# Kernel tuning notes

Measured on AMD Instinct MI355X. Metric: run time of the kernel, lower is better.

The kernel has to match this reference:

```python
import jax, jax.numpy as jnp
import numpy as np

BETA = 0.99
THRESHOLD = 1.0
NUM_STEPS = 100
BATCH = 131072

# snntorch heaviside spike with ATan surrogate gradient (alpha=2 default)
@jax.custom_vjp
def spike(x):
    return (x > 0).astype(x.dtype)

def _spike_fwd(x):
    return (x > 0).astype(x.dtype), x

def _spike_bwd(x, g):
    # d/dx atan surrogate, alpha=2: 1 / (1 + (pi * x)^2)
    return (g / (1.0 + (jnp.pi * x) ** 2),)

spike.defvjp(_spike_fwd, _spike_bwd)


def setup_inputs() -> dict:
    key = jax.random.key(0)
    k = jax.random.split(key, 5)
    x = jax.random.normal(k[0], (BATCH, 2), dtype=jnp.float32)
    # Linear params, fan_in = 2 -> init scale ~ 1/sqrt(2) like torch default
    s = 1.0 / np.sqrt(2.0)
    W1 = jax.random.uniform(k[1], (2, 2), jnp.float32, -s, s)
    b1 = jax.random.uniform(k[2], (2,), jnp.float32, -s, s)
    W2 = jax.random.uniform(k[3], (2, 2), jnp.float32, -s, s)
    b2 = jax.random.uniform(k[4], (2,), jnp.float32, -s, s)
    return {"x": x, "W1": W1, "b1": b1, "W2": W2, "b2": b2}


def reference(x, W1, b1, W2, b2):
    # cur1 = fc1(x) is identical every step; compute once (same math as loop).
    cur1 = x @ W1.T + b1  # [B, 2]

    def lif(mem, cur):
        # snntorch Leaky, reset_mechanism='subtract':
        # reset from PREVIOUS mem (detached), then integrate, then fire.
        reset = jax.lax.stop_gradient((mem - THRESHOLD > 0).astype(mem.dtype))
        mem = BETA * mem + cur - reset * THRESHOLD
        spk = spike(mem - THRESHOLD)
        return spk, mem

    def step(carry, _):
        mem1, mem2 = carry
        spk1, mem1 = lif(mem1, cur1)
        cur2 = spk1 @ W2.T + b2
        spk2, mem2 = lif(mem2, cur2)
        return (mem1, mem2), (spk2, mem2)

    mem0 = jnp.zeros_like(cur1)
    _, (spk2_rec, mem2_rec) = jax.lax.scan(
        step, (mem0, mem0), None, length=NUM_STEPS
    )
    return spk2_rec, mem2_rec  # each [NUM_STEPS, B, 2]
```

## Files before the change

### kernel.cpp

```cpp
#include <hip/hip_runtime.h>

#define BATCH 131072
#define STEPS 100

__global__ __launch_bounds__(256) void snn_lif_kernel(
    const float* __restrict__ x,
    const float* __restrict__ W1, const float* __restrict__ b1,
    const float* __restrict__ W2, const float* __restrict__ b2,
    float* __restrict__ out)
{
    const int tid = blockIdx.x * blockDim.x + threadIdx.x;

    const float w100 = W1[0], w101 = W1[1], w110 = W1[2], w111 = W1[3];
    const float b10  = b1[0], b11  = b1[1];
    const float w200 = W2[0], w201 = W2[1], w210 = W2[2], w211 = W2[3];
    const float b20  = b2[0], b21  = b2[1];

    const float4 xv = reinterpret_cast<const float4*>(x)[tid];

    const float c1a0 = xv.x * w100 + xv.y * w101 + b10;
    const float c1a1 = xv.x * w110 + xv.y * w111 + b11;
    const float c1b0 = xv.z * w100 + xv.w * w101 + b10;
    const float c1b1 = xv.z * w110 + xv.w * w111 + b11;

    float m1a0 = 0.f, m1a1 = 0.f, m1b0 = 0.f, m1b1 = 0.f;
    float m2a0 = 0.f, m2a1 = 0.f, m2b0 = 0.f, m2b1 = 0.f;

    float4* __restrict__ spk_out = reinterpret_cast<float4*>(out);
    float4* __restrict__ mem_out =
        reinterpret_cast<float4*>(out + (size_t)STEPS * BATCH * 2);

    const int slab = BATCH / 2;

#pragma unroll 4
    for (int t = 0; t < STEPS; ++t) {
        float r, s1a0, s1a1, s1b0, s1b1;

        r = (m1a0 > 1.0f) ? 1.0f : 0.0f;
        m1a0 = 0.99f * m1a0 + c1a0 - r;
        s1a0 = (m1a0 > 1.0f) ? 1.0f : 0.0f;

        r = (m1a1 > 1.0f) ? 1.0f : 0.0f;
        m1a1 = 0.99f * m1a1 + c1a1 - r;
        s1a1 = (m1a1 > 1.0f) ? 1.0f : 0.0f;

        r = (m1b0 > 1.0f) ? 1.0f : 0.0f;
        m1b0 = 0.99f * m1b0 + c1b0 - r;
        s1b0 = (m1b0 > 1.0f) ? 1.0f : 0.0f;

        r = (m1b1 > 1.0f) ? 1.0f : 0.0f;
        m1b1 = 0.99f * m1b1 + c1b1 - r;
        s1b1 = (m1b1 > 1.0f) ? 1.0f : 0.0f;

        const float c2a0 = s1a0 * w200 + s1a1 * w201 + b20;
        const float c2a1 = s1a0 * w210 + s1a1 * w211 + b21;
        const float c2b0 = s1b0 * w200 + s1b1 * w201 + b20;
        const float c2b1 = s1b0 * w210 + s1b1 * w211 + b21;

        float4 sp;

        r = (m2a0 > 1.0f) ? 1.0f : 0.0f;
        m2a0 = 0.99f * m2a0 + c2a0 - r;
        sp.x = (m2a0 > 1.0f) ? 1.0f : 0.0f;

        r = (m2a1 > 1.0f) ? 1.0f : 0.0f;
        m2a1 = 0.99f * m2a1 + c2a1 - r;
        sp.y = (m2a1 > 1.0f) ? 1.0f : 0.0f;

        r = (m2b0 > 1.0f) ? 1.0f : 0.0f;
        m2b0 = 0.99f * m2b0 + c2b0 - r;
        sp.z = (m2b0 > 1.0f) ? 1.0f : 0.0f;

        r = (m2b1 > 1.0f) ? 1.0f : 0.0f;
        m2b1 = 0.99f * m2b1 + c2b1 - r;
        sp.w = (m2b1 > 1.0f) ? 1.0f : 0.0f;

        const float4 mm = make_float4(m2a0, m2a1, m2b0, m2b1);

        spk_out[(size_t)t * slab + tid] = sp;
        mem_out[(size_t)t * slab + tid] = mm;
    }
}

extern "C" void kernel_launch(void* const* d_in, const int* in_sizes, int n_in,
                              void* d_out, int out_size, void* d_ws, size_t ws_size,
                              hipStream_t stream) {
    const float* x  = (const float*)d_in[0];
    const float* W1 = (const float*)d_in[1];
    const float* b1 = (const float*)d_in[2];
    const float* W2 = (const float*)d_in[3];
    const float* b2 = (const float*)d_in[4];
    float* out = (float*)d_out;

    const int threads = 256;
    const int blocks = (BATCH / 2) / threads;
    snn_lif_kernel<<<blocks, threads, 0, stream>>>(x, W1, b1, W2, b2, out);
}
```

Before: 35.86 us.

## Split time steps into windows across grid y with recomputed warm-up prefix

The time dimension is split into four windows mapped to blockIdx.y. Each block recomputes the recurrence from step zero up to its window start without storing anything, then writes outputs only for its own window. This quadruples the block count (256 blocks to 1024) so the GPU is filled better and more stores are in flight, at the cost of redundant recurrence compute, up to 75 extra steps for the last window.

```diff
diff --git a/kernel.cpp b/kernel.cpp
--- a/kernel.cpp
+++ b/kernel.cpp
@@ -2,6 +2,42 @@
 
 #define BATCH 131072
 #define STEPS 100
+#define WINDOWS 4
+#define WLEN (STEPS / WINDOWS)
+
+
+#define LIF_STEP()                                                   \
+    do {                                                             \
+        float r, s1a0, s1a1, s1b0, s1b1;                             \
+        r = (m1a0 > 1.0f) ? 1.0f : 0.0f;                             \
+        m1a0 = 0.99f * m1a0 + c1a0 - r;                              \
+        s1a0 = (m1a0 > 1.0f) ? 1.0f : 0.0f;                          \
+        r = (m1a1 > 1.0f) ? 1.0f : 0.0f;                             \
+        m1a1 = 0.99f * m1a1 + c1a1 - r;                              \
+        s1a1 = (m1a1 > 1.0f) ? 1.0f : 0.0f;                          \
+        r = (m1b0 > 1.0f) ? 1.0f : 0.0f;                             \
+        m1b0 = 0.99f * m1b0 + c1b0 - r;                              \
+        s1b0 = (m1b0 > 1.0f) ? 1.0f : 0.0f;                          \
+        r = (m1b1 > 1.0f) ? 1.0f : 0.0f;                             \
+        m1b1 = 0.99f * m1b1 + c1b1 - r;                              \
+        s1b1 = (m1b1 > 1.0f) ? 1.0f : 0.0f;                          \
+        const float c2a0 = s1a0 * w200 + s1a1 * w201 + b20;          \
+        const float c2a1 = s1a0 * w210 + s1a1 * w211 + b21;          \
+        const float c2b0 = s1b0 * w200 + s1b1 * w201 + b20;          \
+        const float c2b1 = s1b0 * w210 + s1b1 * w211 + b21;          \
+        r = (m2a0 > 1.0f) ? 1.0f : 0.0f;                             \
+        m2a0 = 0.99f * m2a0 + c2a0 - r;                              \
+        sp.x = (m2a0 > 1.0f) ? 1.0f : 0.0f;                          \
+        r = (m2a1 > 1.0f) ? 1.0f : 0.0f;                             \
+        m2a1 = 0.99f * m2a1 + c2a1 - r;                              \
+        sp.y = (m2a1 > 1.0f) ? 1.0f : 0.0f;                          \
+        r = (m2b0 > 1.0f) ? 1.0f : 0.0f;                             \
+        m2b0 = 0.99f * m2b0 + c2b0 - r;                              \
+        sp.z = (m2b0 > 1.0f) ? 1.0f : 0.0f;                          \
+        r = (m2b1 > 1.0f) ? 1.0f : 0.0f;                             \
+        m2b1 = 0.99f * m2b1 + c2b1 - r;                              \
+        sp.w = (m2b1 > 1.0f) ? 1.0f : 0.0f;                          \
+    } while (0)
 
 __global__ __launch_bounds__(256) void snn_lif_kernel(
     const float* __restrict__ x,
@@ -10,6 +46,7 @@
     float* __restrict__ out)
 {
     const int tid = blockIdx.x * blockDim.x + threadIdx.x;
+    const int t0 = blockIdx.y * WLEN;
 
     const float w100 = W1[0], w101 = W1[1], w110 = W1[2], w111 = W1[3];
     const float b10  = b1[0], b11  = b1[1];
@@ -32,51 +69,16 @@
 
     const int slab = BATCH / 2;
 
-#pragma unroll 4
-    for (int t = 0; t < STEPS; ++t) {
-        float r, s1a0, s1a1, s1b0, s1b1;
+    float4 sp;
 
-        r = (m1a0 > 1.0f) ? 1.0f : 0.0f;
-        m1a0 = 0.99f * m1a0 + c1a0 - r;
-        s1a0 = (m1a0 > 1.0f) ? 1.0f : 0.0f;
+    for (int t = 0; t < t0; ++t) {
+        LIF_STEP();
+    }
 
-        r = (m1a1 > 1.0f) ? 1.0f : 0.0f;
-        m1a1 = 0.99f * m1a1 + c1a1 - r;
-        s1a1 = (m1a1 > 1.0f) ? 1.0f : 0.0f;
-
-        r = (m1b0 > 1.0f) ? 1.0f : 0.0f;
-        m1b0 = 0.99f * m1b0 + c1b0 - r;
-        s1b0 = (m1b0 > 1.0f) ? 1.0f : 0.0f;
-
-        r = (m1b1 > 1.0f) ? 1.0f : 0.0f;
-        m1b1 = 0.99f * m1b1 + c1b1 - r;
-        s1b1 = (m1b1 > 1.0f) ? 1.0f : 0.0f;
-
-        const float c2a0 = s1a0 * w200 + s1a1 * w201 + b20;
-        const float c2a1 = s1a0 * w210 + s1a1 * w211 + b21;
-        const float c2b0 = s1b0 * w200 + s1b1 * w201 + b20;
-        const float c2b1 = s1b0 * w210 + s1b1 * w211 + b21;
-
-        float4 sp;
-
-        r = (m2a0 > 1.0f) ? 1.0f : 0.0f;
-        m2a0 = 0.99f * m2a0 + c2a0 - r;
-        sp.x = (m2a0 > 1.0f) ? 1.0f : 0.0f;
-
-        r = (m2a1 > 1.0f) ? 1.0f : 0.0f;
-        m2a1 = 0.99f * m2a1 + c2a1 - r;
-        sp.y = (m2a1 > 1.0f) ? 1.0f : 0.0f;
-
-        r = (m2b0 > 1.0f) ? 1.0f : 0.0f;
-        m2b0 = 0.99f * m2b0 + c2b0 - r;
-        sp.z = (m2b0 > 1.0f) ? 1.0f : 0.0f;
-
-        r = (m2b1 > 1.0f) ? 1.0f : 0.0f;
-        m2b1 = 0.99f * m2b1 + c2b1 - r;
-        sp.w = (m2b1 > 1.0f) ? 1.0f : 0.0f;
-
+#pragma unroll 5
+    for (int t = t0; t < t0 + WLEN; ++t) {
+        LIF_STEP();
         const float4 mm = make_float4(m2a0, m2a1, m2b0, m2b1);
-
         spk_out[(size_t)t * slab + tid] = sp;
         mem_out[(size_t)t * slab + tid] = mm;
     }
@@ -93,6 +95,6 @@
     float* out = (float*)d_out;
 
     const int threads = 256;
-    const int blocks = (BATCH / 2) / threads;
-    snn_lif_kernel<<<blocks, threads, 0, stream>>>(x, W1, b1, W2, b2, out);
+    dim3 grid((BATCH / 2) / threads, WINDOWS);
+    snn_lif_kernel<<<grid, threads, 0, stream>>>(x, W1, b1, W2, b2, out);
 }
```

Result: no change. 35.92 us (+0.2%).
